# Kernel tuning notes

Hardware: AMD Instinct MI355X
Metric: run time of the kernel (lower is better)

## Reference

```python
import jax, jax.numpy as jnp
import numpy as np

NUM_GROUPS = 8
EPS = 1e-5


def setup_inputs() -> dict:
    key = jax.random.key(0)
    ks = jax.random.split(key, 4)
    C = 128
    x = jax.random.normal(ks[0], (4, C, 64, 64), dtype=jnp.float32)
    gn_weight = jnp.ones((C,), dtype=jnp.float32)
    gn_bias = jnp.zeros((C,), dtype=jnp.float32)
    qkv_weight = jax.random.normal(ks[1], (3 * C, C), dtype=jnp.float32) * (C ** -0.5)
    qkv_bias = jnp.zeros((3 * C,), dtype=jnp.float32)
    proj_weight = jax.random.normal(ks[2], (C, C), dtype=jnp.float32) * (C ** -0.5)
    proj_bias = jnp.zeros((C,), dtype=jnp.float32)
    return {
        "x": x,
        "gn_weight": gn_weight,
        "gn_bias": gn_bias,
        "qkv_weight": qkv_weight,
        "qkv_bias": qkv_bias,
        "proj_weight": proj_weight,
        "proj_bias": proj_bias,
    }


def reference(x, gn_weight, gn_bias, qkv_weight, qkv_bias, proj_weight, proj_bias):
    b, c, h, w = x.shape
    scale = c ** (-0.5)

    # GroupNorm(8, c): normalize over (channels_in_group, h, w)
    xg = x.reshape(b, NUM_GROUPS, c // NUM_GROUPS, h, w)
    mean = jnp.mean(xg, axis=(2, 3, 4), keepdims=True)
    var = jnp.var(xg, axis=(2, 3, 4), keepdims=True)
    xn = ((xg - mean) * jax.lax.rsqrt(var + EPS)).reshape(b, c, h, w)
    xn = xn * gn_weight[None, :, None, None] + gn_bias[None, :, None, None]

    # 1x1 conv QKV == channel matmul; flatten spatial to sequence n = h*w
    xn_flat = xn.reshape(b, c, h * w)  # [b, c, n]
    qkv = jnp.einsum('oc,bcn->bno', qkv_weight, xn_flat) + qkv_bias  # [b, n, 3c]
    q, k, v = qkv[..., :c], qkv[..., c:2 * c], qkv[..., 2 * c:]

    # attention: materializes [b, n, n] scores as in original
    attn = jnp.einsum('bnc,bmc->bnm', q, k) * scale
    attn = jax.nn.softmax(attn, axis=-1)
    out = jnp.einsum('bnm,bmc->bnc', attn, v)  # [b, n, c]

    # proj 1x1 conv + residual
    out = jnp.einsum('oc,bnc->bno', proj_weight, out) + proj_bias  # [b, n, c]
    out = out.transpose(0, 2, 1).reshape(b, c, h, w)
    return x + out
```

## Files before the change

### kernel.cpp

```cpp
#include <hip/hip_runtime.h>

#define BATCH 4
#define CCH 128
#define NSP 4096
#define NGRP 8
#define GROUP_ELEMS 65536
#define QSCALE 0.12751744f
#define EPS_GN 1e-5f
#define OPSTRIDE 2097152
#define LPSTRIDE 16384

typedef short s8b __attribute__((ext_vector_type(8)));
typedef float f32x4 __attribute__((ext_vector_type(4)));
typedef float f32x16 __attribute__((ext_vector_type(16)));

static __device__ __forceinline__ short f2bf(float f) {
  union { float f; unsigned u; } v; v.f = f;
  unsigned r = (v.u + 0x7FFFu + ((v.u >> 16) & 1u)) >> 16;
  return (short)r;
}

static __device__ __forceinline__ float bf2f(short s) {
  unsigned u = ((unsigned)(unsigned short)s) << 16;
  float f; __builtin_memcpy(&f, &u, 4); return f;
}

static __device__ __forceinline__ float fexp2(float x) {
#if __has_builtin(__builtin_amdgcn_exp2f)
  return __builtin_amdgcn_exp2f(x);
#else
  return exp2f(x);
#endif
}

static __device__ __forceinline__ unsigned pack2bf(float a, float b) {
  unsigned ua, ub;
  __builtin_memcpy(&ua, &a, 4); __builtin_memcpy(&ub, &b, 4);
  ua += 0x8000u; ub += 0x8000u;
#if __has_builtin(__builtin_amdgcn_perm)
  return __builtin_amdgcn_perm(ub, ua, 0x07060302u);
#else
  return (ua >> 16) | (ub & 0xFFFF0000u);
#endif
}

static __device__ __forceinline__ s8b pack8(float a0, float a1, float a2, float a3,
                                            float a4, float a5, float a6, float a7) {
  union { unsigned u[4]; s8b v; } x;
  x.u[0] = pack2bf(a0, a1); x.u[1] = pack2bf(a2, a3);
  x.u[2] = pack2bf(a4, a5); x.u[3] = pack2bf(a6, a7);
  return x.v;
}

static __device__ __forceinline__ f32x4 mfma16(s8b a, s8b b, f32x4 c) {
  return __builtin_amdgcn_mfma_f32_16x16x32_bf16(a, b, c, 0, 0, 0);
}
static __device__ __forceinline__ f32x16 mfma32(s8b a, s8b b, f32x16 c) {
  return __builtin_amdgcn_mfma_f32_32x32x16_bf16(a, b, c, 0, 0, 0);
}

static __device__ __forceinline__ void async16(const void* g, void* l) {
  __builtin_amdgcn_global_load_lds(
      (const __attribute__((address_space(1))) void*)g,
      (__attribute__((address_space(3))) void*)l, 16, 0, 0);
}

__global__ void gn_stats(const float* __restrict__ x, float* __restrict__ part) {
  int bx = blockIdx.x;
  int ch = bx & 7, bg = bx >> 3;
  const float* base = x + (size_t)bg * GROUP_ELEMS + (size_t)ch * 8192;
  int t = threadIdx.x;
  float s = 0.f, ss = 0.f;
  #pragma unroll
  for (int i = 0; i < 8; ++i) {
    float4 v = *(const float4*)(base + i * 1024 + t * 4);
    s  += v.x + v.y + v.z + v.w;
    ss += v.x * v.x + v.y * v.y + v.z * v.z + v.w * v.w;
  }
  #pragma unroll
  for (int off = 1; off < 64; off <<= 1) {
    s  += __shfl_xor(s, off);
    ss += __shfl_xor(ss, off);
  }
  __shared__ float red[8];
  int w = t >> 6;
  if ((t & 63) == 0) { red[w * 2] = s; red[w * 2 + 1] = ss; }
  __syncthreads();
  if (t == 0) {
    part[bx * 2]     = red[0] + red[2] + red[4] + red[6];
    part[bx * 2 + 1] = red[1] + red[3] + red[5] + red[7];
  }
}

__global__ void gn_apply(const float* __restrict__ x, const float* __restrict__ gw,
                         const float* __restrict__ gb, const float* __restrict__ part,
                         short* __restrict__ xn) {
  int bx = blockIdx.x;
  int ns = bx & 7, g = (bx >> 3) & 7, b = bx >> 6;
  int bg = b * NGRP + g;
  float s = 0.f, ss = 0.f;
  #pragma unroll
  for (int j = 0; j < 8; ++j) {
    s  += part[(bg * 8 + j) * 2];
    ss += part[(bg * 8 + j) * 2 + 1];
  }
  float mean = s * (1.f / GROUP_ELEMS);
  float var  = ss * (1.f / GROUP_ELEMS) - mean * mean;
  float inv  = rsqrtf(var + EPS_GN);
  int t = threadIdx.x;
  int cl = t & 15, n4 = t >> 4;
  int c = g * 16 + cl;
  float ga = gw[c] * inv;
  float be = gb[c] - mean * ga;
  const float* xr = x + (size_t)(b * CCH + c) * NSP;
  short* xo = xn + (size_t)b * NSP * CCH + c;
  #pragma unroll
  for (int i = 0; i < 8; ++i) {
    int n = ns * 512 + i * 64 + n4 * 4;
    float4 v = *(const float4*)(xr + n);
    xo[(size_t)(n + 0) * CCH] = f2bf(v.x * ga + be);
    xo[(size_t)(n + 1) * CCH] = f2bf(v.y * ga + be);
    xo[(size_t)(n + 2) * CCH] = f2bf(v.z * ga + be);
    xo[(size_t)(n + 3) * CCH] = f2bf(v.w * ga + be);
  }
}

__global__ void qkv_gemm(const short* __restrict__ xn, const float* __restrict__ Wqkv,
                         const float* __restrict__ bias, short* __restrict__ q,
                         short* __restrict__ k, short* __restrict__ vt) {
  __shared__ short Xl[128 * 136];
  __shared__ short Wl[64 * 136];
  int bx = blockIdx.x;
  int t = threadIdx.x;
  int lane = t & 63, w = t >> 6, l15 = lane & 15, quad = lane >> 4;
  if (bx < 1024) {
    int ot = bx & 3, nt = (bx >> 2) & 63, b = bx >> 8;
    for (int idx = t; idx < 64 * 16; idx += 256) {
      int row = idx >> 4, c8 = idx & 15;
      *(s8b*)&Xl[row * 136 + c8 * 8] =
          *(const s8b*)(xn + ((size_t)(b * NSP + nt * 64 + row)) * CCH + c8 * 8);
    }
    for (int idx = t; idx < 64 * 16; idx += 256) {
      int row = idx >> 4, c8 = idx & 15;
      const float* src = Wqkv + (size_t)(ot * 64 + row) * CCH + c8 * 8;
      s8b wv;
      #pragma unroll
      for (int j = 0; j < 8; ++j) wv[j] = f2bf(src[j]);
      *(s8b*)&Wl[row * 136 + c8 * 8] = wv;
    }
    __syncthreads();
    s8b a[4];
    #pragma unroll
    for (int kc = 0; kc < 4; ++kc)
      a[kc] = *(const s8b*)&Xl[(w * 16 + l15) * 136 + kc * 32 + quad * 8];
    #pragma unroll
    for (int o4 = 0; o4 < 4; ++o4) {
      f32x4 acc = {0.f, 0.f, 0.f, 0.f};
      #pragma unroll
      for (int kc = 0; kc < 4; ++kc) {
        s8b bw = *(const s8b*)&Wl[(o4 * 16 + l15) * 136 + kc * 32 + quad * 8];
        acc = mfma16(a[kc], bw, acc);
      }
      int obase = ot * 64 + o4 * 16;
      short* dst = (obase < 128) ? q : k;
      float mulf = (obase < 128) ? QSCALE : 1.0f;
      int oc = obase - ((obase < 128) ? 0 : 128) + l15;
      float bs = bias[obase + l15];
      #pragma unroll
      for (int r = 0; r < 4; ++r) {
        int n = nt * 64 + w * 16 + quad * 4 + r;
        dst[((size_t)(b * NSP + n)) * CCH + oc] = f2bf((acc[r] + bs) * mulf);
      }
    }
  } else {
    int vbx = bx - 1024;
    int ot = vbx & 1, nt = (vbx >> 1) & 31, b = vbx >> 6;
    for (int idx = t; idx < 128 * 16; idx += 256) {
      int row = idx >> 4, c8 = idx & 15;
      *(s8b*)&Xl[row * 136 + c8 * 8] =
          *(const s8b*)(xn + ((size_t)(b * NSP + nt * 128 + row)) * CCH + c8 * 8);
    }
    for (int idx = t; idx < 64 * 16; idx += 256) {
      int row = idx >> 4, c8 = idx & 15;
      const float* src = Wqkv + (size_t)(256 + ot * 64 + row) * CCH + c8 * 8;
      s8b wv;
      #pragma unroll
      for (int j = 0; j < 8; ++j) wv[j] = f2bf(src[j]);
      *(s8b*)&Wl[row * 136 + c8 * 8] = wv;
    }
    __syncthreads();
    s8b a[4];
    #pragma unroll
    for (int kc = 0; kc < 4; ++kc)
      a[kc] = *(const s8b*)&Wl[(w * 16 + l15) * 136 + kc * 32 + quad * 8];
    float bs[4];
    #pragma unroll
    for (int r = 0; r < 4; ++r) bs[r] = bias[256 + ot * 64 + w * 16 + quad * 4 + r];
    int ppos = 8 * ((l15 >> 2) & 1) + (l15 & 3) + 4 * (l15 >> 3);
    #pragma unroll
    for (int ntile = 0; ntile < 8; ++ntile) {
      f32x4 acc = {0.f, 0.f, 0.f, 0.f};
      #pragma unroll
      for (int kc = 0; kc < 4; ++kc) {
        s8b bx2 = *(const s8b*)&Xl[(ntile * 16 + l15) * 136 + kc * 32 + quad * 8];
        acc = mfma16(a[kc], bx2, acc);
      }
      int npos = nt * 128 + ntile * 16 + ppos;
      #pragma unroll
      for (int r = 0; r < 4; ++r) {
        int og = ot * 64 + w * 16 + quad * 4 + r;
        vt[((size_t)(b * CCH + og)) * NSP + npos] = f2bf(acc[r] + bs[r]);
      }
    }
  }
}

__global__ __launch_bounds__(256, 2) void flash(const short* __restrict__ q,
                                                const short* __restrict__ k,
                                                const short* __restrict__ vt,
                                                short* __restrict__ Op,
                                                float* __restrict__ Lp) {
  int bx = blockIdx.x;
  int kh = bx & 3, b = (bx >> 2) & 3, qt = bx >> 4;
  __shared__ short Kl[2][64 * 128];
  __shared__ short Vl[2][128 * 64];
  int t = threadIdx.x;
  int lane = t & 63, w = t >> 6;
  int l31 = lane & 31, h = lane >> 5;
  const short* kbase = k + (size_t)b * NSP * CCH;
  const short* vbase = vt + (size_t)b * CCH * NSP;
  int kt0 = kh * 1024;

  int krow_in_chunk = lane >> 4, kgrp = lane & 15;
  int vrow_in_chunk = lane >> 3, vgrp = lane & 7;

  s8b aq[8];
  {
    const short* qp = q + ((size_t)(b * NSP + qt * 128 + w * 32 + l31)) * CCH + h * 8;
    #pragma unroll
    for (int kc = 0; kc < 8; ++kc) aq[kc] = *(const s8b*)(qp + kc * 16);
  }
  f32x16 O[4];
  #pragma unroll
  for (int cg = 0; cg < 4; ++cg)
    #pragma unroll
    for (int r = 0; r < 16; ++r) O[cg][r] = 0.f;
  float lsum = 0.f;

  #define STAGE(buf_, key0_)                                                        \
    {                                                                               \
      const int key0v = (key0_);                                                    \
      _Pragma("unroll") for (int si = 0; si < 4; ++si) {                            \
        int c = w * 4 + si;                                                         \
        int rt = c * 4 + krow_in_chunk;                                             \
        async16(kbase + (size_t)(key0v + rt) * CCH + ((kgrp ^ (rt & 15)) * 8),      \
                &Kl[buf_][c * 512]);                                                \
        int rc = c * 8 + vrow_in_chunk;                                             \
        async16(vbase + (size_t)rc * NSP + key0v + ((vgrp ^ (rc & 7)) * 8),         \
                &Vl[buf_][c * 512]);                                                \
      }                                                                             \
    }

  STAGE(0, kt0)
  __syncthreads();

  for (int i = 0; i < 16; ++i) {
    int buf = i & 1;
    if (i < 15) STAGE(buf ^ 1, kt0 + (i + 1) * 64)

    s8b pb[4];
    #pragma unroll
    for (int tile = 0; tile < 2; ++tile) {
      f32x16 st;
      #pragma unroll
      for (int r = 0; r < 16; ++r) st[r] = 0.f;
      const short* kp = &Kl[buf][(tile * 32 + l31) * 128];
      #pragma unroll
      for (int kc = 0; kc < 8; ++kc) {
        s8b ak = *(const s8b*)&kp[(((kc * 2 + h) ^ (l31 & 15))) * 8];
        st = mfma32(ak, aq[kc], st);
      }
      float pp[16];
      #pragma unroll
      for (int r = 0; r < 16; ++r) pp[r] = fexp2(st[r]);
      lsum += (((pp[0] + pp[1]) + (pp[2] + pp[3])) + ((pp[4] + pp[5]) + (pp[6] + pp[7]))) +
              (((pp[8] + pp[9]) + (pp[10] + pp[11])) + ((pp[12] + pp[13]) + (pp[14] + pp[15])));
      pb[tile * 2 + 0] = pack8(pp[0], pp[1], pp[2], pp[3], pp[4], pp[5], pp[6], pp[7]);
      pb[tile * 2 + 1] = pack8(pp[8], pp[9], pp[10], pp[11], pp[12], pp[13], pp[14], pp[15]);
    }
    #pragma unroll
    for (int cg = 0; cg < 4; ++cg) {
      const short* vp = &Vl[buf][(cg * 32 + l31) * 64];
      #pragma unroll
      for (int kc2 = 0; kc2 < 4; ++kc2) {
        s8b av = *(const s8b*)&vp[(((kc2 * 2 + h) ^ (l31 & 7))) * 8];
        O[cg] = mfma32(av, pb[kc2], O[cg]);
      }
    }
    __syncthreads();
  }

  lsum += __shfl_xor(lsum, 32);

  short* eb = &Kl[0][0] + w * 4096;
  #pragma unroll
  for (int cg = 0; cg < 4; ++cg)
    #pragma unroll
    for (int rp = 0; rp < 8; ++rp) {
      int r = rp * 2;
      int chlo = (r & 3) + 4 * h;
      int chhi = cg * 4 + (r >> 2);
      *(unsigned*)&eb[l31 * 128 + ((chhi ^ (l31 & 7))) * 8 + chlo] =
          pack2bf(O[cg][r], O[cg][r + 1]);
    }
  short* ob = Op + (size_t)kh * OPSTRIDE + ((size_t)(b * NSP + qt * 128)) * CCH;
  float* lp = Lp + kh * LPSTRIDE + b * NSP + qt * 128;
  if (lane < 32) lp[w * 32 + l31] = lsum;
  __syncthreads();
  for (int idx = t; idx < 128 * 16; idx += 256) {
    int row = idx >> 4, c8 = idx & 15;
    int w2 = row >> 5, nl = row & 31;
    *(s8b*)(ob + (size_t)row * CCH + c8 * 8) =
        *(const s8b*)(&Kl[0][0] + w2 * 4096 + nl * 128 + ((c8 ^ (nl & 7))) * 8);
  }
}

__global__ void proj_gemm(const short* __restrict__ Op, const float* __restrict__ Lp,
                          const float* __restrict__ Wp, const float* __restrict__ pbias,
                          const float* __restrict__ x, float* __restrict__ out) {
  int bx = blockIdx.x;
  int nt = bx & 63, b = bx >> 6;
  __shared__ short Wl[128][136];
  int t = threadIdx.x;
  for (int idx = t; idx < 128 * 16; idx += 256) {
    int row = idx >> 4, c8 = idx & 15;
    const float* src = Wp + (size_t)row * CCH + c8 * 8;
    s8b wv;
    #pragma unroll
    for (int j = 0; j < 8; ++j) wv[j] = f2bf(src[j]);
    *(s8b*)&Wl[row][c8 * 8] = wv;
  }
  __syncthreads();
  int lane = t & 63, w = t >> 6, l15 = lane & 15, quad = lane >> 4;
  int row = nt * 64 + w * 16 + l15;
  float lsum = Lp[0 * LPSTRIDE + b * NSP + row] + Lp[1 * LPSTRIDE + b * NSP + row] +
               Lp[2 * LPSTRIDE + b * NSP + row] + Lp[3 * LPSTRIDE + b * NSP + row];
  float linv = 1.f / lsum;
  const short* ap = Op + ((size_t)(b * NSP + row)) * CCH + quad * 8;
  s8b bfr[4];
  #pragma unroll
  for (int kc = 0; kc < 4; ++kc) {
    float acc8[8];
    #pragma unroll
    for (int j = 0; j < 8; ++j) acc8[j] = 0.f;
    #pragma unroll
    for (int s = 0; s < 4; ++s) {
      s8b tv = *(const s8b*)(ap + (size_t)s * OPSTRIDE + kc * 32);
      #pragma unroll
      for (int j = 0; j < 8; ++j) acc8[j] += bf2f(tv[j]);
    }
    #pragma unroll
    for (int j = 0; j < 8; ++j) bfr[kc][j] = f2bf(acc8[j] * linv);
  }
  #pragma unroll
  for (int cg = 0; cg < 8; ++cg) {
    f32x4 acc = {0.f, 0.f, 0.f, 0.f};
    #pragma unroll
    for (int kc = 0; kc < 4; ++kc) {
      s8b aw = *(const s8b*)&Wl[cg * 16 + l15][kc * 32 + quad * 8];
      acc = mfma16(aw, bfr[kc], acc);
    }
    #pragma unroll
    for (int r = 0; r < 4; ++r) {
      int co = cg * 16 + quad * 4 + r;
      int n = nt * 64 + w * 16 + l15;
      size_t off = ((size_t)(b * CCH + co)) * NSP + n;
      out[off] = x[off] + acc[r] + pbias[co];
    }
  }
}

extern "C" void kernel_launch(void* const* d_in, const int* in_sizes, int n_in,
                              void* d_out, int out_size, void* d_ws, size_t ws_size,
                              hipStream_t stream) {
  (void)in_sizes; (void)n_in; (void)out_size; (void)ws_size;
  const float* x    = (const float*)d_in[0];
  const float* gw   = (const float*)d_in[1];
  const float* gb   = (const float*)d_in[2];
  const float* Wqkv = (const float*)d_in[3];
  const float* bqkv = (const float*)d_in[4];
  const float* Wp   = (const float*)d_in[5];
  const float* bp   = (const float*)d_in[6];
  float* out = (float*)d_out;
  char* ws = (char*)d_ws;
  float* part = (float*)ws;
  short* xn    = (short*)(ws + 4096);
  short* q     = (short*)(ws + 4096 + 1ull * 4194304);
  short* k     = (short*)(ws + 4096 + 2ull * 4194304);
  short* vt    = (short*)(ws + 4096 + 3ull * 4194304);
  short* Opart = (short*)(ws + 4096 + 4ull * 4194304);
  float* Lpart = (float*)(ws + 4096 + 8ull * 4194304);

  gn_stats<<<256, 256, 0, stream>>>(x, part);
  gn_apply<<<256, 256, 0, stream>>>(x, gw, gb, part, xn);
  qkv_gemm<<<1280, 256, 0, stream>>>(xn, Wqkv, bqkv, q, k, vt);
  flash<<<512, 256, 0, stream>>>(q, k, vt, Opart, Lpart);
  proj_gemm<<<256, 256, 0, stream>>>(Opart, Lpart, Wp, bp, x, out);
}
```

Baseline: 133.8 us.

## Double query rows per flash wave and split keys eight ways

```diff
diff --git a/kernel.cpp b/kernel.cpp
--- a/kernel.cpp
+++ b/kernel.cpp
@@ -7,6 +7,7 @@
 #define GROUP_ELEMS 65536
 #define QSCALE 0.12751744f
 #define EPS_GN 1e-5f
+#define KHN 8
 #define OPSTRIDE 2097152
 #define LPSTRIDE 16384
 
@@ -33,22 +34,17 @@
 #endif
 }
 
-static __device__ __forceinline__ unsigned pack2bf(float a, float b) {
-  unsigned ua, ub;
-  __builtin_memcpy(&ua, &a, 4); __builtin_memcpy(&ub, &b, 4);
-  ua += 0x8000u; ub += 0x8000u;
-#if __has_builtin(__builtin_amdgcn_perm)
-  return __builtin_amdgcn_perm(ub, ua, 0x07060302u);
-#else
-  return (ua >> 16) | (ub & 0xFFFF0000u);
-#endif
+static __device__ __forceinline__ unsigned cvtpk(float a, float b) {
+  unsigned r;
+  asm("v_cvt_pk_bf16_f32 %0, %1, %2" : "=v"(r) : "v"(a), "v"(b));
+  return r;
 }
 
 static __device__ __forceinline__ s8b pack8(float a0, float a1, float a2, float a3,
                                             float a4, float a5, float a6, float a7) {
   union { unsigned u[4]; s8b v; } x;
-  x.u[0] = pack2bf(a0, a1); x.u[1] = pack2bf(a2, a3);
-  x.u[2] = pack2bf(a4, a5); x.u[3] = pack2bf(a6, a7);
+  x.u[0] = cvtpk(a0, a1); x.u[1] = cvtpk(a2, a3);
+  x.u[2] = cvtpk(a4, a5); x.u[3] = cvtpk(a6, a7);
   return x.v;
 }
 
@@ -221,31 +217,36 @@
                                                 short* __restrict__ Op,
                                                 float* __restrict__ Lp) {
   int bx = blockIdx.x;
-  int kh = bx & 3, b = (bx >> 2) & 3, qt = bx >> 4;
-  __shared__ short Kl[2][64 * 128];
-  __shared__ short Vl[2][128 * 64];
+  int kh = bx & 7, b = (bx >> 3) & 3, qt = bx >> 5;
+  __shared__ short lds[32768];
+  short* Kl = lds;
+  short* Vl = lds + 16384;
   int t = threadIdx.x;
   int lane = t & 63, w = t >> 6;
   int l31 = lane & 31, h = lane >> 5;
+  int x15 = l31 & 15, x7 = l31 & 7;
   const short* kbase = k + (size_t)b * NSP * CCH;
   const short* vbase = vt + (size_t)b * CCH * NSP;
-  int kt0 = kh * 1024;
+  int kt0 = kh * 512;
 
   int krow_in_chunk = lane >> 4, kgrp = lane & 15;
   int vrow_in_chunk = lane >> 3, vgrp = lane & 7;
 
-  s8b aq[8];
+  s8b aq0[8], aq1[8];
   {
-    const short* qp = q + ((size_t)(b * NSP + qt * 128 + w * 32 + l31)) * CCH + h * 8;
-    #pragma unroll
-    for (int kc = 0; kc < 8; ++kc) aq[kc] = *(const s8b*)(qp + kc * 16);
-  }
-  f32x16 O[4];
+    const short* qp = q + ((size_t)(b * NSP + qt * 256 + w * 64 + l31)) * CCH + h * 8;
+    #pragma unroll
+    for (int kc = 0; kc < 8; ++kc) aq0[kc] = *(const s8b*)(qp + kc * 16);
+    qp += (size_t)32 * CCH;
+    #pragma unroll
+    for (int kc = 0; kc < 8; ++kc) aq1[kc] = *(const s8b*)(qp + kc * 16);
+  }
+  f32x16 O0[4], O1[4];
   #pragma unroll
   for (int cg = 0; cg < 4; ++cg)
     #pragma unroll
-    for (int r = 0; r < 16; ++r) O[cg][r] = 0.f;
-  float lsum = 0.f;
+    for (int r = 0; r < 16; ++r) { O0[cg][r] = 0.f; O1[cg][r] = 0.f; }
+  float lsum0 = 0.f, lsum1 = 0.f;
 
   #define STAGE(buf_, key0_)                                                        \
     {                                                                               \
@@ -254,55 +255,74 @@
         int c = w * 4 + si;                                                         \
         int rt = c * 4 + krow_in_chunk;                                             \
         async16(kbase + (size_t)(key0v + rt) * CCH + ((kgrp ^ (rt & 15)) * 8),      \
-                &Kl[buf_][c * 512]);                                                \
+                Kl + (buf_) * 8192 + c * 512);                                      \
         int rc = c * 8 + vrow_in_chunk;                                             \
         async16(vbase + (size_t)rc * NSP + key0v + ((vgrp ^ (rc & 7)) * 8),         \
-                &Vl[buf_][c * 512]);                                                \
+                Vl + (buf_) * 8192 + c * 512);                                      \
       }                                                                             \
     }
 
   STAGE(0, kt0)
   __syncthreads();
 
-  for (int i = 0; i < 16; ++i) {
+  for (int i = 0; i < 8; ++i) {
     int buf = i & 1;
-    if (i < 15) STAGE(buf ^ 1, kt0 + (i + 1) * 64)
-
-    s8b pb[4];
+    if (i < 7) STAGE(buf ^ 1, kt0 + (i + 1) * 64)
+    int bo = buf * 8192;
+
+    s8b pb0[4], pb1[4];
     #pragma unroll
     for (int tile = 0; tile < 2; ++tile) {
-      f32x16 st;
-      #pragma unroll
-      for (int r = 0; r < 16; ++r) st[r] = 0.f;
-      const short* kp = &Kl[buf][(tile * 32 + l31) * 128];
+      f32x16 st0, st1;
+      #pragma unroll
+      for (int r = 0; r < 16; ++r) { st0[r] = 0.f; st1[r] = 0.f; }
+      const short* kp = Kl + bo + (tile * 32 + l31) * 128;
+      __builtin_amdgcn_s_setprio(1);
       #pragma unroll
       for (int kc = 0; kc < 8; ++kc) {
-        s8b ak = *(const s8b*)&kp[(((kc * 2 + h) ^ (l31 & 15))) * 8];
-        st = mfma32(ak, aq[kc], st);
-      }
-      float pp[16];
-      #pragma unroll
-      for (int r = 0; r < 16; ++r) pp[r] = fexp2(st[r]);
-      lsum += (((pp[0] + pp[1]) + (pp[2] + pp[3])) + ((pp[4] + pp[5]) + (pp[6] + pp[7]))) +
-              (((pp[8] + pp[9]) + (pp[10] + pp[11])) + ((pp[12] + pp[13]) + (pp[14] + pp[15])));
-      pb[tile * 2 + 0] = pack8(pp[0], pp[1], pp[2], pp[3], pp[4], pp[5], pp[6], pp[7]);
-      pb[tile * 2 + 1] = pack8(pp[8], pp[9], pp[10], pp[11], pp[12], pp[13], pp[14], pp[15]);
-    }
+        s8b ak = *(const s8b*)&kp[((kc * 2 + h) ^ x15) * 8];
+        st0 = mfma32(ak, aq0[kc], st0);
+        st1 = mfma32(ak, aq1[kc], st1);
+      }
+      __builtin_amdgcn_s_setprio(0);
+      {
+        float p[16];
+        #pragma unroll
+        for (int r = 0; r < 16; ++r) p[r] = fexp2(st0[r]);
+        lsum0 += (((p[0] + p[1]) + (p[2] + p[3])) + ((p[4] + p[5]) + (p[6] + p[7]))) +
+                 (((p[8] + p[9]) + (p[10] + p[11])) + ((p[12] + p[13]) + (p[14] + p[15])));
+        pb0[tile * 2 + 0] = pack8(p[0], p[1], p[2], p[3], p[4], p[5], p[6], p[7]);
+        pb0[tile * 2 + 1] = pack8(p[8], p[9], p[10], p[11], p[12], p[13], p[14], p[15]);
+      }
+      {
+        float p[16];
+        #pragma unroll
+        for (int r = 0; r < 16; ++r) p[r] = fexp2(st1[r]);
+        lsum1 += (((p[0] + p[1]) + (p[2] + p[3])) + ((p[4] + p[5]) + (p[6] + p[7]))) +
+                 (((p[8] + p[9]) + (p[10] + p[11])) + ((p[12] + p[13]) + (p[14] + p[15])));
+        pb1[tile * 2 + 0] = pack8(p[0], p[1], p[2], p[3], p[4], p[5], p[6], p[7]);
+        pb1[tile * 2 + 1] = pack8(p[8], p[9], p[10], p[11], p[12], p[13], p[14], p[15]);
+      }
+    }
+    __builtin_amdgcn_s_setprio(1);
     #pragma unroll
     for (int cg = 0; cg < 4; ++cg) {
-      const short* vp = &Vl[buf][(cg * 32 + l31) * 64];
+      const short* vp = Vl + bo + (cg * 32 + l31) * 64;
       #pragma unroll
       for (int kc2 = 0; kc2 < 4; ++kc2) {
-        s8b av = *(const s8b*)&vp[(((kc2 * 2 + h) ^ (l31 & 7))) * 8];
-        O[cg] = mfma32(av, pb[kc2], O[cg]);
-      }
-    }
+        s8b av = *(const s8b*)&vp[((kc2 * 2 + h) ^ x7) * 8];
+        O0[cg] = mfma32(av, pb0[kc2], O0[cg]);
+        O1[cg] = mfma32(av, pb1[kc2], O1[cg]);
+      }
+    }
+    __builtin_amdgcn_s_setprio(0);
     __syncthreads();
   }
 
-  lsum += __shfl_xor(lsum, 32);
-
-  short* eb = &Kl[0][0] + w * 4096;
+  lsum0 += __shfl_xor(lsum0, 32);
+  lsum1 += __shfl_xor(lsum1, 32);
+
+  short* eb = lds + w * 8192;
   #pragma unroll
   for (int cg = 0; cg < 4; ++cg)
     #pragma unroll
@@ -310,18 +330,18 @@
       int r = rp * 2;
       int chlo = (r & 3) + 4 * h;
       int chhi = cg * 4 + (r >> 2);
-      *(unsigned*)&eb[l31 * 128 + ((chhi ^ (l31 & 7))) * 8 + chlo] =
-          pack2bf(O[cg][r], O[cg][r + 1]);
-    }
-  short* ob = Op + (size_t)kh * OPSTRIDE + ((size_t)(b * NSP + qt * 128)) * CCH;
-  float* lp = Lp + kh * LPSTRIDE + b * NSP + qt * 128;
-  if (lane < 32) lp[w * 32 + l31] = lsum;
+      *(unsigned*)&eb[l31 * 128 + ((chhi ^ x7)) * 8 + chlo] = cvtpk(O0[cg][r], O0[cg][r + 1]);
+      *(unsigned*)&eb[4096 + l31 * 128 + ((chhi ^ x7)) * 8 + chlo] = cvtpk(O1[cg][r], O1[cg][r + 1]);
+    }
+  short* ob = Op + (size_t)kh * OPSTRIDE + ((size_t)(b * NSP + qt * 256)) * CCH;
+  float* lp = Lp + kh * LPSTRIDE + b * NSP + qt * 256;
+  if (lane < 32) { lp[w * 64 + l31] = lsum0; lp[w * 64 + 32 + l31] = lsum1; }
   __syncthreads();
-  for (int idx = t; idx < 128 * 16; idx += 256) {
+  for (int idx = t; idx < 256 * 16; idx += 256) {
     int row = idx >> 4, c8 = idx & 15;
-    int w2 = row >> 5, nl = row & 31;
+    int w2 = row >> 6, sub = (row >> 5) & 1, nl = row & 31;
     *(s8b*)(ob + (size_t)row * CCH + c8 * 8) =
-        *(const s8b*)(&Kl[0][0] + w2 * 4096 + nl * 128 + ((c8 ^ (nl & 7))) * 8);
+        *(const s8b*)(lds + w2 * 8192 + sub * 4096 + nl * 128 + ((c8 ^ (nl & 7))) * 8);
   }
 }
 
@@ -343,8 +363,9 @@
   __syncthreads();
   int lane = t & 63, w = t >> 6, l15 = lane & 15, quad = lane >> 4;
   int row = nt * 64 + w * 16 + l15;
-  float lsum = Lp[0 * LPSTRIDE + b * NSP + row] + Lp[1 * LPSTRIDE + b * NSP + row] +
-               Lp[2 * LPSTRIDE + b * NSP + row] + Lp[3 * LPSTRIDE + b * NSP + row];
+  float lsum = 0.f;
+  #pragma unroll
+  for (int s = 0; s < KHN; ++s) lsum += Lp[(size_t)s * LPSTRIDE + b * NSP + row];
   float linv = 1.f / lsum;
   const short* ap = Op + ((size_t)(b * NSP + row)) * CCH + quad * 8;
   s8b bfr[4];
@@ -354,7 +375,7 @@
     #pragma unroll
     for (int j = 0; j < 8; ++j) acc8[j] = 0.f;
     #pragma unroll
-    for (int s = 0; s < 4; ++s) {
+    for (int s = 0; s < KHN; ++s) {
       s8b tv = *(const s8b*)(ap + (size_t)s * OPSTRIDE + kc * 32);
       #pragma unroll
       for (int j = 0; j < 8; ++j) acc8[j] += bf2f(tv[j]);
@@ -399,7 +420,7 @@
   short* k     = (short*)(ws + 4096 + 2ull * 4194304);
   short* vt    = (short*)(ws + 4096 + 3ull * 4194304);
   short* Opart = (short*)(ws + 4096 + 4ull * 4194304);
-  float* Lpart = (float*)(ws + 4096 + 8ull * 4194304);
+  float* Lpart = (float*)(ws + 4096 + 12ull * 4194304);
 
   gn_stats<<<256, 256, 0, stream>>>(x, part);
   gn_apply<<<256, 256, 0, stream>>>(x, gw, gb, part, xn);
```

Result: slower. 273.5 us (+104.4%).
